# Kernel tuning notes

Hardware: AMD Instinct MI355X
Metric: run time of the kernel (lower is better)

The kernel has to match this reference:

```python
import jax, jax.numpy as jnp
import numpy as np
import math

H = 8
D_MODEL = 512
D_K = D_MODEL // H
DIM_G = 64
WAVE_LEN = 1000.0


def box_relational_embedding(f_g):
    # f_g: [B, N, 4] -> [B, N, N, 64] trigonometric geometry embedding
    x_min, y_min, x_max, y_max = jnp.split(f_g, 4, axis=-1)  # each [B,N,1]
    cx = (x_min + x_max) * 0.5
    cy = (y_min + y_max) * 0.5
    w = x_max - x_min + 1.0
    h = y_max - y_min + 1.0
    # pairwise deltas: [B,N,1] vs [B,1,N] -> [B,N,N]
    cx_t = jnp.swapaxes(cx, 1, 2)  # [B,1,N]
    cy_t = jnp.swapaxes(cy, 1, 2)
    w_t = jnp.swapaxes(w, 1, 2)
    h_t = jnp.swapaxes(h, 1, 2)
    delta_x = jnp.log(jnp.maximum(jnp.abs((cx - cx_t) / w), 0.001))
    delta_y = jnp.log(jnp.maximum(jnp.abs((cy - cy_t) / h), 0.001))
    delta_w = jnp.log(w / w_t)
    delta_h = jnp.log(h / h_t)
    position_mat = jnp.stack([delta_x, delta_y, delta_w, delta_h], axis=-1)  # [B,N,N,4]
    feat_range = jnp.arange(DIM_G // 8, dtype=position_mat.dtype) / (DIM_G / 8)
    dim_mat = 1.0 / jnp.power(jnp.asarray(WAVE_LEN, position_mat.dtype), feat_range)  # [8]
    mul_mat = (100.0 * position_mat)[..., None] * dim_mat  # [B,N,N,4,8]
    B, N = position_mat.shape[0], position_mat.shape[1]
    mul_mat = mul_mat.reshape(B, N, N, -1)  # [B,N,N,32]
    return jnp.concatenate([jnp.sin(mul_mat), jnp.cos(mul_mat)], axis=-1)  # [B,N,N,64]


def setup_inputs() -> dict:
    key = jax.random.key(0)
    ks = jax.random.split(key, 16)
    B, N = 16, 256
    scale = 1.0 / math.sqrt(D_MODEL)
    inp = {
        'input_query': jax.random.normal(ks[0], (B, N, D_MODEL), jnp.float32),
        'input_key': jax.random.normal(ks[1], (B, N, D_MODEL), jnp.float32),
        'input_value': jax.random.normal(ks[2], (B, N, D_MODEL), jnp.float32),
        'input_box': jax.random.uniform(ks[3], (B, N, 4), jnp.float32),
        'mask': jnp.ones((B, N), jnp.int32),
        # projection weights stored as [d_in, d_out] (x @ W + b)
        'Wq': jax.random.normal(ks[4], (D_MODEL, D_MODEL), jnp.float32) * scale,
        'bq': jnp.zeros((D_MODEL,), jnp.float32),
        'Wk': jax.random.normal(ks[5], (D_MODEL, D_MODEL), jnp.float32) * scale,
        'bk': jnp.zeros((D_MODEL,), jnp.float32),
        'Wv': jax.random.normal(ks[6], (D_MODEL, D_MODEL), jnp.float32) * scale,
        'bv': jnp.zeros((D_MODEL,), jnp.float32),
        'Wo': jax.random.normal(ks[7], (D_MODEL, D_MODEL), jnp.float32) * scale,
        'bo': jnp.zeros((D_MODEL,), jnp.float32),
        # 8 geometric-bias heads: Linear(64 -> 1) each, stacked -> [H, 64], [H]
        'WG_w': jax.random.normal(ks[8], (H, DIM_G), jnp.float32) * (1.0 / math.sqrt(DIM_G)),
        'WG_b': jnp.zeros((H,), jnp.float32),
    }
    return inp


def reference(input_query, input_key, input_value, input_box, mask,
              Wq, bq, Wk, bk, Wv, bv, Wo, bo, WG_w, WG_b):
    B, N, _ = input_query.shape

    def proj(x, W, b):  # [B,N,D] -> [B,H,N,d_k]
        return (x @ W + b).reshape(B, N, H, D_K).transpose(0, 2, 1, 3)

    q = proj(input_query, Wq, bq)
    k = proj(input_key, Wk, bk)
    v = proj(input_value, Wv, bv)

    geo = box_relational_embedding(input_box)  # [B,N,N,64]
    # per-head geometric weights, ReLU'd: [B,H,N,N]
    w_g = jax.nn.relu(jnp.einsum('bnmg,hg->bhnm', geo, WG_w) + WG_b[None, :, None, None])

    scaled_dot = jnp.einsum('bhqd,bhkd->bhqk', q, k) / np.sqrt(D_K).astype(q.dtype)
    # mask: [B,N] keys -> [B,1,1,N], broadcast over heads and queries
    scaled_dot = jnp.where(mask[:, None, None, :] == 0, jnp.asarray(-1e9, scaled_dot.dtype), scaled_dot)
    w_mn = jax.nn.softmax(jnp.log(jnp.maximum(w_g, 1e-6)) + scaled_dot, axis=-1)
    # dropout is identity in eval mode
    out = jnp.einsum('bhqk,bhkd->bhqd', w_mn, v)  # [B,H,N,d_k]
    out = out.transpose(0, 2, 1, 3).reshape(B, N, H * D_K)
    return out @ Wo + bo
```

## Files before the change

### kernel.cpp

```cpp
#include <hip/hip_runtime.h>
#include <hip/hip_fp16.h>
#include <math.h>

#define Bv   16
#define Nv   256
#define Dv   512
#define Hv   8
#define MNv  4096

typedef __attribute__((ext_vector_type(8))) short bf16x8;
typedef __attribute__((ext_vector_type(4))) float f32x4;
typedef __fp16 fp16x8 __attribute__((ext_vector_type(8)));
typedef __fp16 fp16x2 __attribute__((ext_vector_type(2)));

__device__ __forceinline__ unsigned short f2bf(float f) {
    unsigned u = __float_as_uint(f);
    u = u + 0x7FFFu + ((u >> 16) & 1u);
    return (unsigned short)(u >> 16);
}
__device__ __forceinline__ void gload_lds16(const void* g, void* l) {
    __builtin_amdgcn_global_load_lds(
        (const __attribute__((address_space(1))) unsigned int*)g,
        (__attribute__((address_space(3))) unsigned int*)l, 16, 0, 0);
}

__device__ __forceinline__ void fast_sincos(float x, float* s, float* c) {
    const float rev = x * 0.15915494309189535f;
    const float fr  = rev - floorf(rev);
    *s = __builtin_amdgcn_sinf(fr);
    *c = __builtin_amdgcn_cosf(fr);
}

__global__ __launch_bounds__(256) void conv_b16_kernel(
    const float* __restrict__ xq, const float* __restrict__ xk,
    const float* __restrict__ xv, unsigned short* __restrict__ Ab)
{
    const int z = blockIdx.z;
    const float* src = (z == 0) ? xq : (z == 1) ? xk : xv;
    const size_t base = (size_t)z * (MNv * Dv);
    const int idx = (blockIdx.x * 256 + threadIdx.x) * 4;
    float4 x = *(const float4*)(src + idx);
    ushort4 h;
    h.x = f2bf(x.x); h.y = f2bf(x.y); h.z = f2bf(x.z); h.w = f2bf(x.w);
    *(ushort4*)(Ab + base + idx) = h;
}

__global__ __launch_bounds__(256) void conv_w_kernel(
    const float* __restrict__ Wq, const float* __restrict__ Wk,
    const float* __restrict__ Wv, const float* __restrict__ Wo,
    const float* __restrict__ bq, const float* __restrict__ bk,
    const float* __restrict__ bv, const float* __restrict__ bo,
    unsigned short* __restrict__ Wt, float* __restrict__ biasStack)
{
    const int z = blockIdx.z;
    const float* W = (z == 0) ? Wq : (z == 1) ? Wk : (z == 2) ? Wv : Wo;
    const float* b = (z == 0) ? bq : (z == 1) ? bk : (z == 2) ? bv : bo;
    const int n0 = blockIdx.x * 64, k0 = blockIdx.y * 64;
    const int t = threadIdx.x;
    __shared__ float T[64][65];
    const int col = t & 63, rb = t >> 6;
#pragma unroll
    for (int i = 0; i < 16; ++i) {
        const int row = i * 4 + rb;
        T[row][col] = W[(k0 + row) * Dv + n0 + col];
    }
    __syncthreads();
#pragma unroll
    for (int i = 0; i < 16; ++i) {
        const int row = i * 4 + rb;
        Wt[z * (Dv * Dv) + (n0 + row) * Dv + k0 + col] = f2bf(T[col][row]);
    }
    if (blockIdx.x == 0 && blockIdx.y == 0) {
        biasStack[z * Dv + t]       = b[t];
        biasStack[z * Dv + t + 256] = b[t + 256];
    }
}

__global__ __launch_bounds__(256) void qkv_gemm_kernel(
    const unsigned short* __restrict__ Ab, const unsigned short* __restrict__ Wt,
    const float* __restrict__ bst, unsigned short* __restrict__ Qb2,
    unsigned short* __restrict__ Kb2, unsigned short* __restrict__ Vt2)
{
    const int z = blockIdx.z;
    const unsigned short* A = Ab + (size_t)z * (MNv * Dv);
    const unsigned short* Wz = Wt + (size_t)z * (Dv * Dv);
    const float* bias = bst + z * Dv;

    const int n0 = blockIdx.x * 128;
    const int m0 = blockIdx.y * 128;
    const int t = threadIdx.x;
    const int w = t >> 6, lane = t & 63;
    const int wm = w & 1, wn = w >> 1;

    __shared__ unsigned short As[128][32];
    __shared__ unsigned short Bs[128][32];

    f32x4 acc[4][4] = {};

    const int sr = lane >> 2;
    const int sk = (lane & 3) * 8;
    const int fr = lane & 15;
    const int fk = (lane >> 4) * 8;

    for (int k0 = 0; k0 < Dv; k0 += 32) {
        __syncthreads();
#pragma unroll
        for (int j = 0; j < 2; ++j) {
            const int row = w * 32 + j * 16 + sr;
            gload_lds16(A  + (size_t)(m0 + row) * Dv + k0 + sk, &As[w * 32 + j * 16][0]);
            gload_lds16(Wz + (size_t)(n0 + row) * Dv + k0 + sk, &Bs[w * 32 + j * 16][0]);
        }
        __syncthreads();

        bf16x8 af[4], bfr[4];
#pragma unroll
        for (int mt = 0; mt < 4; ++mt)
            af[mt] = *(const bf16x8*)&As[wm * 64 + mt * 16 + fr][fk];
#pragma unroll
        for (int nt = 0; nt < 4; ++nt)
            bfr[nt] = *(const bf16x8*)&Bs[wn * 64 + nt * 16 + fr][fk];
#pragma unroll
        for (int mt = 0; mt < 4; ++mt)
#pragma unroll
            for (int nt = 0; nt < 4; ++nt)
                acc[mt][nt] = __builtin_amdgcn_mfma_f32_16x16x32_bf16(
                    af[mt], bfr[nt], acc[mt][nt], 0, 0, 0);
    }

    const int er = (lane >> 4) * 4;
    const int ec = lane & 15;
    const float scale = (z == 0) ? 0.125f : 1.0f;
#pragma unroll
    for (int nt = 0; nt < 4; ++nt) {
        const int gn = n0 + wn * 64 + nt * 16 + ec;
        const float bv_ = bias[gn];
#pragma unroll
        for (int mt = 0; mt < 4; ++mt) {
            const int gm = m0 + wm * 64 + mt * 16 + er;
            if (z == 2) {
                ushort4 o;
                o.x = f2bf(acc[mt][nt][0] + bv_);
                o.y = f2bf(acc[mt][nt][1] + bv_);
                o.z = f2bf(acc[mt][nt][2] + bv_);
                o.w = f2bf(acc[mt][nt][3] + bv_);
                *(ushort4*)(Vt2 + ((size_t)(gm >> 8) * Dv + gn) * Nv + (gm & 255)) = o;
            } else {
                unsigned short* cp = ((z == 0) ? Qb2 : Kb2) + (size_t)gm * Dv + gn;
#pragma unroll
                for (int r = 0; r < 4; ++r)
                    cp[(size_t)r * Dv] = f2bf((acc[mt][nt][r] + bv_) * scale);
            }
        }
    }
}

__global__ __launch_bounds__(256) void out_gemm_kernel(
    const unsigned short* __restrict__ A, const unsigned short* __restrict__ Wz,
    const float* __restrict__ bias, float* __restrict__ C)
{
    const int n0 = blockIdx.x * 64;
    const int m0 = blockIdx.y * 128;
    const int t = threadIdx.x;
    const int w = t >> 6, lane = t & 63;
    const int wm = w & 1, wn = w >> 1;

    __shared__ unsigned short As[128][32];
    __shared__ unsigned short Bs[64][32];

    f32x4 acc[4][2] = {};

    const int sr = lane >> 2;
    const int sk = (lane & 3) * 8;
    const int fr = lane & 15;
    const int fk = (lane >> 4) * 8;

    for (int k0 = 0; k0 < Dv; k0 += 32) {
        __syncthreads();
#pragma unroll
        for (int j = 0; j < 2; ++j) {
            const int row = w * 32 + j * 16 + sr;
            gload_lds16(A + (size_t)(m0 + row) * Dv + k0 + sk, &As[w * 32 + j * 16][0]);
        }
        gload_lds16(Wz + (size_t)(n0 + w * 16 + sr) * Dv + k0 + sk, &Bs[w * 16][0]);
        __syncthreads();

        bf16x8 af[4], bfr[2];
#pragma unroll
        for (int mt = 0; mt < 4; ++mt)
            af[mt] = *(const bf16x8*)&As[wm * 64 + mt * 16 + fr][fk];
#pragma unroll
        for (int nt = 0; nt < 2; ++nt)
            bfr[nt] = *(const bf16x8*)&Bs[wn * 32 + nt * 16 + fr][fk];
#pragma unroll
        for (int mt = 0; mt < 4; ++mt)
#pragma unroll
            for (int nt = 0; nt < 2; ++nt)
                acc[mt][nt] = __builtin_amdgcn_mfma_f32_16x16x32_bf16(
                    af[mt], bfr[nt], acc[mt][nt], 0, 0, 0);
    }

    const int er = (lane >> 4) * 4;
    const int ec = lane & 15;
#pragma unroll
    for (int nt = 0; nt < 2; ++nt) {
        const int gn = n0 + wn * 32 + nt * 16 + ec;
        const float bv_ = bias[gn];
#pragma unroll
        for (int mt = 0; mt < 4; ++mt) {
            const int gm = m0 + wm * 64 + mt * 16 + er;
            float* cp = C + (size_t)gm * Dv + gn;
#pragma unroll
            for (int r = 0; r < 4; ++r)
                cp[(size_t)r * Dv] = acc[mt][nt][r] + bv_;
        }
    }
}

__global__ __launch_bounds__(256) void geo_mfma_kernel(
    const float* __restrict__ box, const int* __restrict__ mask,
    const float* __restrict__ WGw, const float* __restrict__ WGb,
    __half* __restrict__ LB)
{
    const int q = blockIdx.x;
    const int b = blockIdx.y;
    const int t = threadIdx.x;
    const int w = t >> 6, lane = t & 63;
    const int n = lane & 15;
    const int quad = lane >> 4;

    __shared__ unsigned short Lst[Hv][264];

    const float4 bq_ = *(const float4*)(box + (b * Nv + q) * 4);
    const float cxq = (bq_.x + bq_.z) * 0.5f;
    const float cyq = (bq_.y + bq_.w) * 0.5f;
    const float wq  = bq_.z - bq_.x + 1.0f;
    const float hq  = bq_.w - bq_.y + 1.0f;

    union F16x8 { fp16x8 v; fp16x2 p[4]; };
    F16x8 Bs_, Bc_;
    Bs_.v = (fp16x8){}; Bc_.v = (fp16x8){};
    float bias_n = 0.0f;
    if (n < Hv) {
        bias_n = WGb[n];
#pragma unroll
        for (int jj = 0; jj < 4; ++jj) {
            Bs_.p[jj] = __builtin_amdgcn_cvt_pkrtz(WGw[n * 64 + quad * 8 + 2 * jj],
                                                   WGw[n * 64 + quad * 8 + 2 * jj + 1]);
            Bc_.p[jj] = __builtin_amdgcn_cvt_pkrtz(WGw[n * 64 + 32 + quad * 8 + 2 * jj],
                                                   WGw[n * 64 + 32 + quad * 8 + 2 * jj + 1]);
        }
    }

    const float dimm[8] = {1.0f, 0.42169650342f, 0.17782794100f, 0.07498942093f,
                           0.03162277660f, 0.01333521432f, 0.00562341325f, 0.00237137371f};
    const bool isCtr = (quad < 2);
    const bool isY   = (quad & 1);
    const float cq  = isY ? cyq : cxq;
    const float sq_ = isY ? hq : wq;

#pragma unroll
    for (int i = 0; i < 4; ++i) {
        const int m0 = (w * 4 + i) * 16;
        const float4 bm = *(const float4*)(box + (b * Nv + m0 + n) * 4);
        const float cxm = (bm.x + bm.z) * 0.5f;
        const float cym = (bm.y + bm.w) * 0.5f;
        const float wm  = bm.z - bm.x + 1.0f;
        const float hm  = bm.w - bm.y + 1.0f;
        const float cm_ = isY ? cym : cxm;
        const float sm_ = isY ? hm : wm;
        const float top = isCtr ? fabsf(cq - cm_) : sq_;
        const float bot = isCtr ? sq_ : sm_;
        float r = top / bot;
        if (isCtr) r = fmaxf(r, 1e-3f);
        const float base = 100.0f * __logf(r);

        float sv[8], cv[8];
#pragma unroll
        for (int j = 0; j < 8; ++j)
            fast_sincos(base * dimm[j], &sv[j], &cv[j]);

        F16x8 As_, Ac_;
#pragma unroll
        for (int jj = 0; jj < 4; ++jj) {
            As_.p[jj] = __builtin_amdgcn_cvt_pkrtz(sv[2 * jj], sv[2 * jj + 1]);
            Ac_.p[jj] = __builtin_amdgcn_cvt_pkrtz(cv[2 * jj], cv[2 * jj + 1]);
        }

        f32x4 acc = {};
        acc = __builtin_amdgcn_mfma_f32_16x16x32_f16(As_.v, Bs_.v, acc, 0, 0, 0);
        acc = __builtin_amdgcn_mfma_f32_16x16x32_f16(Ac_.v, Bc_.v, acc, 0, 0, 0);

        const int mrow = m0 + quad * 4;
        const int4 mk = *(const int4*)(mask + b * Nv + mrow);
        if (n < Hv) {
            const int* mkp = (const int*)&mk;
            const int pos0 = quad * 64 + (w * 4 + i);
#pragma unroll
            for (int rr = 0; rr < 4; ++rr) {
                const float val = fmaxf(acc[rr] + bias_n, 1e-6f);
                const float lb = __logf(val) + (mkp[rr] ? 0.0f : -30000.0f);
                Lst[n][pos0 + rr * 16] = __half_as_ushort(__float2half(lb));
            }
        }
    }

    __syncthreads();

    const int h = t >> 5, c = t & 31;
    unsigned short* dst = (unsigned short*)LB +
                          ((size_t)(b * Hv + h) * Nv + q) * Nv + c * 8;
    *(int4*)dst = *(const int4*)&Lst[h][c * 8];
}

__global__ __launch_bounds__(256) void attn3_kernel(
    const unsigned short* __restrict__ Qb2, const unsigned short* __restrict__ Kb2,
    const unsigned short* __restrict__ Vt2, const __half* __restrict__ LB,
    unsigned short* __restrict__ CTXb)
{
    const int qt = blockIdx.x, h = blockIdx.y, b = blockIdx.z;
    const int q0 = qt * 64;
    const int t = threadIdx.x, w = t >> 6, lane = t & 63;
    const int fr = lane & 15, fq = lane >> 4;

    __shared__ unsigned short Qs[64][72];
    __shared__ unsigned short Ks[256][72];
    __shared__ unsigned short Vt[64][264];
    unsigned short (*Pb)[264] = (unsigned short (*)[264])&Ks[0][0];

#pragma unroll
    for (int i = 0; i < 2; ++i) {
        const int idx = t + i * 256;
        const int row = idx >> 3, cu = idx & 7;
        *(bf16x8*)&Qs[row][cu * 8] =
            *(const bf16x8*)(Qb2 + (size_t)(b * Nv + q0 + row) * Dv + h * 64 + cu * 8);
    }
#pragma unroll
    for (int i = 0; i < 8; ++i) {
        const int idx = t + i * 256;
        const int row = idx >> 3, cu = idx & 7;
        *(bf16x8*)&Ks[row][cu * 8] =
            *(const bf16x8*)(Kb2 + (size_t)(b * Nv + row) * Dv + h * 64 + cu * 8);
    }
#pragma unroll
    for (int i = 0; i < 8; ++i) {
        const int idx = t + i * 256;
        const int row = idx >> 5, cu = idx & 31;
        *(bf16x8*)&Vt[row][cu * 8] =
            *(const bf16x8*)(Vt2 + (size_t)b * (Dv * Nv) + (h * 64 + row) * Nv + cu * 8);
    }

    f32x4 acc[16];
    const int qb = q0 + w * 16 + fq * 4;
    const __half* lbp = LB + ((size_t)(b * Hv + h) * Nv + qb) * Nv + fr * 16;
#pragma unroll
    for (int r = 0; r < 4; ++r) {
        union { int4 v; __half hs[8]; } u0, u1;
        const int4* p = (const int4*)(lbp + (size_t)r * Nv);
        u0.v = p[0]; u1.v = p[1];
#pragma unroll
        for (int nt = 0; nt < 8; ++nt) acc[nt][r]     = __half2float(u0.hs[nt]);
#pragma unroll
        for (int nt = 0; nt < 8; ++nt) acc[nt + 8][r] = __half2float(u1.hs[nt]);
    }

    __syncthreads();

    const bf16x8 aq0 = *(const bf16x8*)&Qs[w * 16 + fr][fq * 8];
    const bf16x8 aq1 = *(const bf16x8*)&Qs[w * 16 + fr][32 + fq * 8];
#pragma unroll
    for (int nt = 0; nt < 16; ++nt) {
        const bf16x8 bk0 = *(const bf16x8*)&Ks[nt * 16 + fr][fq * 8];
        const bf16x8 bk1 = *(const bf16x8*)&Ks[nt * 16 + fr][32 + fq * 8];
        acc[nt] = __builtin_amdgcn_mfma_f32_16x16x32_bf16(aq0, bk0, acc[nt], 0, 0, 0);
        acc[nt] = __builtin_amdgcn_mfma_f32_16x16x32_bf16(aq1, bk1, acc[nt], 0, 0, 0);
    }

    float ri[4];
#pragma unroll
    for (int r = 0; r < 4; ++r) {
        float mx = acc[0][r];
#pragma unroll
        for (int nt = 1; nt < 16; ++nt) mx = fmaxf(mx, acc[nt][r]);
        mx = fmaxf(mx, __shfl_xor(mx, 1));
        mx = fmaxf(mx, __shfl_xor(mx, 2));
        mx = fmaxf(mx, __shfl_xor(mx, 4));
        mx = fmaxf(mx, __shfl_xor(mx, 8));
        float s = 0.0f;
#pragma unroll
        for (int nt = 0; nt < 16; ++nt) {
            const float e = __expf(acc[nt][r] - mx);
            acc[nt][r] = e;
            s += e;
        }
        s += __shfl_xor(s, 1);
        s += __shfl_xor(s, 2);
        s += __shfl_xor(s, 4);
        s += __shfl_xor(s, 8);
        ri[r] = 1.0f / s;
    }

    __syncthreads();

#pragma unroll
    for (int nt = 0; nt < 16; ++nt)
#pragma unroll
        for (int r = 0; r < 4; ++r)
            Pb[w * 16 + fq * 4 + r][nt * 16 + fr] = f2bf(acc[nt][r] * ri[r]);

    f32x4 o[4] = {};
#pragma unroll
    for (int kt = 0; kt < 8; ++kt) {
        const bf16x8 ap = *(const bf16x8*)&Pb[w * 16 + fr][kt * 32 + fq * 8];
#pragma unroll
        for (int nt2 = 0; nt2 < 4; ++nt2) {
            const bf16x8 bv_ = *(const bf16x8*)&Vt[nt2 * 16 + fr][kt * 32 + fq * 8];
            o[nt2] = __builtin_amdgcn_mfma_f32_16x16x32_bf16(ap, bv_, o[nt2], 0, 0, 0);
        }
    }

#pragma unroll
    for (int nt2 = 0; nt2 < 4; ++nt2)
#pragma unroll
        for (int r = 0; r < 4; ++r)
            CTXb[(size_t)(b * Nv + qb + r) * Dv + h * 64 + nt2 * 16 + fr] =
                f2bf(o[nt2][r]);
}

extern "C" void kernel_launch(void* const* d_in, const int* in_sizes, int n_in,
                              void* d_out, int out_size, void* d_ws, size_t ws_size,
                              hipStream_t stream) {
    (void)in_sizes; (void)n_in; (void)out_size; (void)ws_size;

    const float* inq  = (const float*)d_in[0];
    const float* ink  = (const float*)d_in[1];
    const float* inv  = (const float*)d_in[2];
    const float* box  = (const float*)d_in[3];
    const int*   mask = (const int*)d_in[4];
    const float* Wq   = (const float*)d_in[5];
    const float* bq   = (const float*)d_in[6];
    const float* Wk   = (const float*)d_in[7];
    const float* bk   = (const float*)d_in[8];
    const float* Wv   = (const float*)d_in[9];
    const float* bv   = (const float*)d_in[10];
    const float* Wo   = (const float*)d_in[11];
    const float* bo   = (const float*)d_in[12];
    const float* WGw  = (const float*)d_in[13];
    const float* WGb  = (const float*)d_in[14];

    char* W = (char*)d_ws;
    const size_t MB = 1048576;
    unsigned short* Qb2  = (unsigned short*)(W + 0);
    unsigned short* Kb2  = (unsigned short*)(W + 4 * MB);
    unsigned short* Vt2  = (unsigned short*)(W + 8 * MB);
    unsigned short* Wt   = (unsigned short*)(W + 12 * MB);
    float*          bst  = (float*)(W + 14 * MB);
    unsigned short* CTXb = (unsigned short*)(W + 15 * MB);
    unsigned short* Ab   = (unsigned short*)(W + 20 * MB);
    __half*         LB   = (__half*)(W + 20 * MB);

    float* out = (float*)d_out;

    conv_b16_kernel<<<dim3(2048, 1, 3), 256, 0, stream>>>(inq, ink, inv, Ab);
    conv_w_kernel<<<dim3(8, 8, 4), 256, 0, stream>>>(Wq, Wk, Wv, Wo, bq, bk, bv, bo, Wt, bst);

    qkv_gemm_kernel<<<dim3(4, 32, 3), 256, 0, stream>>>(Ab, Wt, bst, Qb2, Kb2, Vt2);

    geo_mfma_kernel<<<dim3(Nv, Bv), 256, 0, stream>>>(box, mask, WGw, WGb, LB);

    attn3_kernel<<<dim3(4, 8, 16), 256, 0, stream>>>(Qb2, Kb2, Vt2, LB, CTXb);

    out_gemm_kernel<<<dim3(8, 32), 256, 0, stream>>>(CTXb, Wt + 3 * (Dv * Dv), bst + 3 * Dv, out);
}
```

Measured before the change: 169.0 us.

## Merge geometry, input conversion and weight transpose into one launch; shrink QKV GEMM tile

Three independent preprocessing kernels (geometry bias, bf16 input conversion, weight transpose/convert) are merged into one block-indexed kernel, and the geometry output buffer moves to its own workspace region so it no longer aliases the converted inputs. The goal is to cut launch overhead and let the geometry work overlap with the memory-bound conversion. The QKV GEMM tile is narrowed from 128 to 64 columns, doubling the grid to 768 blocks for better CU occupancy, at the cost of less B-tile reuse per block.

```diff
diff --git a/kernel.cpp b/kernel.cpp
--- a/kernel.cpp
+++ b/kernel.cpp
@@ -31,48 +31,146 @@
     *c = __builtin_amdgcn_cosf(fr);
 }
 
-__global__ __launch_bounds__(256) void conv_b16_kernel(
+__global__ __launch_bounds__(256) void mega1_kernel(
+    const float* __restrict__ box, const int* __restrict__ mask,
+    const float* __restrict__ WGw, const float* __restrict__ WGb,
+    __half* __restrict__ LB,
     const float* __restrict__ xq, const float* __restrict__ xk,
-    const float* __restrict__ xv, unsigned short* __restrict__ Ab)
-{
-    const int z = blockIdx.z;
-    const float* src = (z == 0) ? xq : (z == 1) ? xk : xv;
-    const size_t base = (size_t)z * (MNv * Dv);
-    const int idx = (blockIdx.x * 256 + threadIdx.x) * 4;
-    float4 x = *(const float4*)(src + idx);
-    ushort4 h;
-    h.x = f2bf(x.x); h.y = f2bf(x.y); h.z = f2bf(x.z); h.w = f2bf(x.w);
-    *(ushort4*)(Ab + base + idx) = h;
-}
-
-__global__ __launch_bounds__(256) void conv_w_kernel(
+    const float* __restrict__ xv, unsigned short* __restrict__ Ab,
     const float* __restrict__ Wq, const float* __restrict__ Wk,
     const float* __restrict__ Wv, const float* __restrict__ Wo,
     const float* __restrict__ bq, const float* __restrict__ bk,
     const float* __restrict__ bv, const float* __restrict__ bo,
     unsigned short* __restrict__ Wt, float* __restrict__ biasStack)
 {
-    const int z = blockIdx.z;
-    const float* W = (z == 0) ? Wq : (z == 1) ? Wk : (z == 2) ? Wv : Wo;
-    const float* b = (z == 0) ? bq : (z == 1) ? bk : (z == 2) ? bv : bo;
-    const int n0 = blockIdx.x * 64, k0 = blockIdx.y * 64;
+    __shared__ __align__(16) char smraw[64 * 65 * 4];
+    const int bid = blockIdx.x;
     const int t = threadIdx.x;
-    __shared__ float T[64][65];
-    const int col = t & 63, rb = t >> 6;
-#pragma unroll
-    for (int i = 0; i < 16; ++i) {
-        const int row = i * 4 + rb;
-        T[row][col] = W[(k0 + row) * Dv + n0 + col];
-    }
-    __syncthreads();
-#pragma unroll
-    for (int i = 0; i < 16; ++i) {
-        const int row = i * 4 + rb;
-        Wt[z * (Dv * Dv) + (n0 + row) * Dv + k0 + col] = f2bf(T[col][row]);
-    }
-    if (blockIdx.x == 0 && blockIdx.y == 0) {
-        biasStack[z * Dv + t]       = b[t];
-        biasStack[z * Dv + t + 256] = b[t + 256];
+
+    if (bid < 4096) {
+        unsigned short (*Lst)[264] = (unsigned short (*)[264])smraw;
+        const int q = bid & 255;
+        const int b = bid >> 8;
+        const int w = t >> 6, lane = t & 63;
+        const int n = lane & 15;
+        const int quad = lane >> 4;
+
+        const float4 bq_ = *(const float4*)(box + (b * Nv + q) * 4);
+        const float cxq = (bq_.x + bq_.z) * 0.5f;
+        const float cyq = (bq_.y + bq_.w) * 0.5f;
+        const float wq  = bq_.z - bq_.x + 1.0f;
+        const float hq  = bq_.w - bq_.y + 1.0f;
+
+        union F16x8 { fp16x8 v; fp16x2 p[4]; };
+        F16x8 Bs_, Bc_;
+        Bs_.v = (fp16x8){}; Bc_.v = (fp16x8){};
+        float bias_n = 0.0f;
+        if (n < Hv) {
+            bias_n = WGb[n];
+#pragma unroll
+            for (int jj = 0; jj < 4; ++jj) {
+                Bs_.p[jj] = __builtin_amdgcn_cvt_pkrtz(WGw[n * 64 + quad * 8 + 2 * jj],
+                                                       WGw[n * 64 + quad * 8 + 2 * jj + 1]);
+                Bc_.p[jj] = __builtin_amdgcn_cvt_pkrtz(WGw[n * 64 + 32 + quad * 8 + 2 * jj],
+                                                       WGw[n * 64 + 32 + quad * 8 + 2 * jj + 1]);
+            }
+        }
+
+        const float dimm[8] = {1.0f, 0.42169650342f, 0.17782794100f, 0.07498942093f,
+                               0.03162277660f, 0.01333521432f, 0.00562341325f, 0.00237137371f};
+        const bool isCtr = (quad < 2);
+        const bool isY   = (quad & 1);
+        const float cq  = isY ? cyq : cxq;
+        const float sq_ = isY ? hq : wq;
+
+#pragma unroll
+        for (int i = 0; i < 4; ++i) {
+            const int m0 = (w * 4 + i) * 16;
+            const float4 bm = *(const float4*)(box + (b * Nv + m0 + n) * 4);
+            const float cxm = (bm.x + bm.z) * 0.5f;
+            const float cym = (bm.y + bm.w) * 0.5f;
+            const float wm  = bm.z - bm.x + 1.0f;
+            const float hm  = bm.w - bm.y + 1.0f;
+            const float cm_ = isY ? cym : cxm;
+            const float sm_ = isY ? hm : wm;
+            const float top = isCtr ? fabsf(cq - cm_) : sq_;
+            const float bot = isCtr ? sq_ : sm_;
+            float r = top / bot;
+            if (isCtr) r = fmaxf(r, 1e-3f);
+            const float base = 100.0f * __logf(r);
+
+            float sv[8], cv[8];
+#pragma unroll
+            for (int j = 0; j < 8; ++j)
+                fast_sincos(base * dimm[j], &sv[j], &cv[j]);
+
+            F16x8 As_, Ac_;
+#pragma unroll
+            for (int jj = 0; jj < 4; ++jj) {
+                As_.p[jj] = __builtin_amdgcn_cvt_pkrtz(sv[2 * jj], sv[2 * jj + 1]);
+                Ac_.p[jj] = __builtin_amdgcn_cvt_pkrtz(cv[2 * jj], cv[2 * jj + 1]);
+            }
+
+            f32x4 acc = {};
+            acc = __builtin_amdgcn_mfma_f32_16x16x32_f16(As_.v, Bs_.v, acc, 0, 0, 0);
+            acc = __builtin_amdgcn_mfma_f32_16x16x32_f16(Ac_.v, Bc_.v, acc, 0, 0, 0);
+
+            const int mrow = m0 + quad * 4;
+            const int4 mk = *(const int4*)(mask + b * Nv + mrow);
+            if (n < Hv) {
+                const int* mkp = (const int*)&mk;
+                const int pos0 = quad * 64 + (w * 4 + i);
+#pragma unroll
+                for (int rr = 0; rr < 4; ++rr) {
+                    const float val = fmaxf(acc[rr] + bias_n, 1e-6f);
+                    const float lb = __logf(val) + (mkp[rr] ? 0.0f : -30000.0f);
+                    Lst[n][pos0 + rr * 16] = __half_as_ushort(__float2half(lb));
+                }
+            }
+        }
+
+        __syncthreads();
+        const int h = t >> 5, c = t & 31;
+        unsigned short* dst = (unsigned short*)LB +
+                              ((size_t)(b * Hv + h) * Nv + q) * Nv + c * 8;
+        *(int4*)dst = *(const int4*)&Lst[h][c * 8];
+
+    } else if (bid < 10240) {
+        const int i = bid - 4096;
+        const int z = i >> 11;
+        const int xblk = i & 2047;
+        const float* src = (z == 0) ? xq : (z == 1) ? xk : xv;
+        const size_t base = (size_t)z * (MNv * Dv);
+        const int idx = (xblk * 256 + t) * 4;
+        float4 x = *(const float4*)(src + idx);
+        ushort4 h4;
+        h4.x = f2bf(x.x); h4.y = f2bf(x.y); h4.z = f2bf(x.z); h4.w = f2bf(x.w);
+        *(ushort4*)(Ab + base + idx) = h4;
+
+    } else {
+        float (*T)[65] = (float (*)[65])smraw;
+        const int i = bid - 10240;
+        const int z = i >> 6;
+        const int rem = i & 63;
+        const int n0 = (rem & 7) * 64, k0 = (rem >> 3) * 64;
+        const float* W = (z == 0) ? Wq : (z == 1) ? Wk : (z == 2) ? Wv : Wo;
+        const float* b = (z == 0) ? bq : (z == 1) ? bk : (z == 2) ? bv : bo;
+        const int col = t & 63, rb = t >> 6;
+#pragma unroll
+        for (int j = 0; j < 16; ++j) {
+            const int row = j * 4 + rb;
+            T[row][col] = W[(k0 + row) * Dv + n0 + col];
+        }
+        __syncthreads();
+#pragma unroll
+        for (int j = 0; j < 16; ++j) {
+            const int row = j * 4 + rb;
+            Wt[z * (Dv * Dv) + (n0 + row) * Dv + k0 + col] = f2bf(T[col][row]);
+        }
+        if (rem == 0) {
+            biasStack[z * Dv + t]       = b[t];
+            biasStack[z * Dv + t + 256] = b[t + 256];
+        }
     }
 }
 
@@ -86,16 +184,16 @@
     const unsigned short* Wz = Wt + (size_t)z * (Dv * Dv);
     const float* bias = bst + z * Dv;
 
-    const int n0 = blockIdx.x * 128;
+    const int n0 = blockIdx.x * 64;
     const int m0 = blockIdx.y * 128;
     const int t = threadIdx.x;
     const int w = t >> 6, lane = t & 63;
     const int wm = w & 1, wn = w >> 1;
 
     __shared__ unsigned short As[128][32];
-    __shared__ unsigned short Bs[128][32];
-
-    f32x4 acc[4][4] = {};
+    __shared__ unsigned short Bs[64][32];
+
+    f32x4 acc[4][2] = {};
 
     const int sr = lane >> 2;
     const int sk = (lane & 3) * 8;
@@ -107,22 +205,22 @@
 #pragma unroll
         for (int j = 0; j < 2; ++j) {
             const int row = w * 32 + j * 16 + sr;
-            gload_lds16(A  + (size_t)(m0 + row) * Dv + k0 + sk, &As[w * 32 + j * 16][0]);
-            gload_lds16(Wz + (size_t)(n0 + row) * Dv + k0 + sk, &Bs[w * 32 + j * 16][0]);
-        }
-        __syncthreads();
-
-        bf16x8 af[4], bfr[4];
+            gload_lds16(A + (size_t)(m0 + row) * Dv + k0 + sk, &As[w * 32 + j * 16][0]);
+        }
+        gload_lds16(Wz + (size_t)(n0 + w * 16 + sr) * Dv + k0 + sk, &Bs[w * 16][0]);
+        __syncthreads();
+
+        bf16x8 af[4], bfr[2];
 #pragma unroll
         for (int mt = 0; mt < 4; ++mt)
             af[mt] = *(const bf16x8*)&As[wm * 64 + mt * 16 + fr][fk];
 #pragma unroll
-        for (int nt = 0; nt < 4; ++nt)
-            bfr[nt] = *(const bf16x8*)&Bs[wn * 64 + nt * 16 + fr][fk];
+        for (int nt = 0; nt < 2; ++nt)
+            bfr[nt] = *(const bf16x8*)&Bs[wn * 32 + nt * 16 + fr][fk];
 #pragma unroll
         for (int mt = 0; mt < 4; ++mt)
 #pragma unroll
-            for (int nt = 0; nt < 4; ++nt)
+            for (int nt = 0; nt < 2; ++nt)
                 acc[mt][nt] = __builtin_amdgcn_mfma_f32_16x16x32_bf16(
                     af[mt], bfr[nt], acc[mt][nt], 0, 0, 0);
     }
@@ -131,8 +229,8 @@
     const int ec = lane & 15;
     const float scale = (z == 0) ? 0.125f : 1.0f;
 #pragma unroll
-    for (int nt = 0; nt < 4; ++nt) {
-        const int gn = n0 + wn * 64 + nt * 16 + ec;
+    for (int nt = 0; nt < 2; ++nt) {
+        const int gn = n0 + wn * 32 + nt * 16 + ec;
         const float bv_ = bias[gn];
 #pragma unroll
         for (int mt = 0; mt < 4; ++mt) {
@@ -214,102 +312,6 @@
                 cp[(size_t)r * Dv] = acc[mt][nt][r] + bv_;
         }
     }
-}
-
-__global__ __launch_bounds__(256) void geo_mfma_kernel(
-    const float* __restrict__ box, const int* __restrict__ mask,
-    const float* __restrict__ WGw, const float* __restrict__ WGb,
-    __half* __restrict__ LB)
-{
-    const int q = blockIdx.x;
-    const int b = blockIdx.y;
-    const int t = threadIdx.x;
-    const int w = t >> 6, lane = t & 63;
-    const int n = lane & 15;
-    const int quad = lane >> 4;
-
-    __shared__ unsigned short Lst[Hv][264];
-
-    const float4 bq_ = *(const float4*)(box + (b * Nv + q) * 4);
-    const float cxq = (bq_.x + bq_.z) * 0.5f;
-    const float cyq = (bq_.y + bq_.w) * 0.5f;
-    const float wq  = bq_.z - bq_.x + 1.0f;
-    const float hq  = bq_.w - bq_.y + 1.0f;
-
-    union F16x8 { fp16x8 v; fp16x2 p[4]; };
-    F16x8 Bs_, Bc_;
-    Bs_.v = (fp16x8){}; Bc_.v = (fp16x8){};
-    float bias_n = 0.0f;
-    if (n < Hv) {
-        bias_n = WGb[n];
-#pragma unroll
-        for (int jj = 0; jj < 4; ++jj) {
-            Bs_.p[jj] = __builtin_amdgcn_cvt_pkrtz(WGw[n * 64 + quad * 8 + 2 * jj],
-                                                   WGw[n * 64 + quad * 8 + 2 * jj + 1]);
-            Bc_.p[jj] = __builtin_amdgcn_cvt_pkrtz(WGw[n * 64 + 32 + quad * 8 + 2 * jj],
-                                                   WGw[n * 64 + 32 + quad * 8 + 2 * jj + 1]);
-        }
-    }
-
-    const float dimm[8] = {1.0f, 0.42169650342f, 0.17782794100f, 0.07498942093f,
-                           0.03162277660f, 0.01333521432f, 0.00562341325f, 0.00237137371f};
-    const bool isCtr = (quad < 2);
-    const bool isY   = (quad & 1);
-    const float cq  = isY ? cyq : cxq;
-    const float sq_ = isY ? hq : wq;
-
-#pragma unroll
-    for (int i = 0; i < 4; ++i) {
-        const int m0 = (w * 4 + i) * 16;
-        const float4 bm = *(const float4*)(box + (b * Nv + m0 + n) * 4);
-        const float cxm = (bm.x + bm.z) * 0.5f;
-        const float cym = (bm.y + bm.w) * 0.5f;
-        const float wm  = bm.z - bm.x + 1.0f;
-        const float hm  = bm.w - bm.y + 1.0f;
-        const float cm_ = isY ? cym : cxm;
-        const float sm_ = isY ? hm : wm;
-        const float top = isCtr ? fabsf(cq - cm_) : sq_;
-        const float bot = isCtr ? sq_ : sm_;
-        float r = top / bot;
-        if (isCtr) r = fmaxf(r, 1e-3f);
-        const float base = 100.0f * __logf(r);
-
-        float sv[8], cv[8];
-#pragma unroll
-        for (int j = 0; j < 8; ++j)
-            fast_sincos(base * dimm[j], &sv[j], &cv[j]);
-
-        F16x8 As_, Ac_;
-#pragma unroll
-        for (int jj = 0; jj < 4; ++jj) {
-            As_.p[jj] = __builtin_amdgcn_cvt_pkrtz(sv[2 * jj], sv[2 * jj + 1]);
-            Ac_.p[jj] = __builtin_amdgcn_cvt_pkrtz(cv[2 * jj], cv[2 * jj + 1]);
-        }
-
-        f32x4 acc = {};
-        acc = __builtin_amdgcn_mfma_f32_16x16x32_f16(As_.v, Bs_.v, acc, 0, 0, 0);
-        acc = __builtin_amdgcn_mfma_f32_16x16x32_f16(Ac_.v, Bc_.v, acc, 0, 0, 0);
-
-        const int mrow = m0 + quad * 4;
-        const int4 mk = *(const int4*)(mask + b * Nv + mrow);
-        if (n < Hv) {
-            const int* mkp = (const int*)&mk;
-            const int pos0 = quad * 64 + (w * 4 + i);
-#pragma unroll
-            for (int rr = 0; rr < 4; ++rr) {
-                const float val = fmaxf(acc[rr] + bias_n, 1e-6f);
-                const float lb = __logf(val) + (mkp[rr] ? 0.0f : -30000.0f);
-                Lst[n][pos0 + rr * 16] = __half_as_ushort(__float2half(lb));
-            }
-        }
-    }
-
-    __syncthreads();
-
-    const int h = t >> 5, c = t & 31;
-    unsigned short* dst = (unsigned short*)LB +
-                          ((size_t)(b * Hv + h) * Nv + q) * Nv + c * 8;
-    *(int4*)dst = *(const int4*)&Lst[h][c * 8];
 }
 
 __global__ __launch_bounds__(256) void attn3_kernel(
@@ -456,16 +458,15 @@
     float*          bst  = (float*)(W + 14 * MB);
     unsigned short* CTXb = (unsigned short*)(W + 15 * MB);
     unsigned short* Ab   = (unsigned short*)(W + 20 * MB);
-    __half*         LB   = (__half*)(W + 20 * MB);
-
+    __half*         LB   = (__half*)(W + 32 * MB);
     float* out = (float*)d_out;
 
-    conv_b16_kernel<<<dim3(2048, 1, 3), 256, 0, stream>>>(inq, ink, inv, Ab);
-    conv_w_kernel<<<dim3(8, 8, 4), 256, 0, stream>>>(Wq, Wk, Wv, Wo, bq, bk, bv, bo, Wt, bst);
-
-    qkv_gemm_kernel<<<dim3(4, 32, 3), 256, 0, stream>>>(Ab, Wt, bst, Qb2, Kb2, Vt2);
-
-    geo_mfma_kernel<<<dim3(Nv, Bv), 256, 0, stream>>>(box, mask, WGw, WGb, LB);
+    mega1_kernel<<<10496, 256, 0, stream>>>(
+        box, mask, WGw, WGb, LB,
+        inq, ink, inv, Ab,
+        Wq, Wk, Wv, Wo, bq, bk, bv, bo, Wt, bst);
+
+    qkv_gemm_kernel<<<dim3(8, 32, 3), 256, 0, stream>>>(Ab, Wt, bst, Qb2, Kb2, Vt2);
 
     attn3_kernel<<<dim3(4, 8, 16), 256, 0, stream>>>(Qb2, Kb2, Vt2, LB, CTXb);
 
```

Result: faster. 161.1 us (-4.7%).
